# Kernel optimization log

Hardware: AMD Instinct MI355X
Metric: run time of the kernel (lower is better)

## Reference

```python
import jax, jax.numpy as jnp
import numpy as np

N = 50000
E = 800000
T = 10
H = 128
D = 64
P = 65536


def setup_inputs() -> dict:
    key = jax.random.key(0)
    ks = jax.random.split(key, 16)
    inp = {}
    inp["node_type_ids"] = jax.random.randint(ks[0], (N,), 0, T)
    inp["adj_rows"] = jax.random.randint(ks[1], (E,), 0, N)
    inp["adj_cols"] = jax.random.randint(ks[2], (E,), 0, N)
    inp["adj_vals"] = jax.random.uniform(ks[3], (E,), dtype=jnp.float32)
    inp["pairs"] = jax.random.randint(ks[4], (2, P), 0, N)
    s = 0.02
    inp["node_emb"] = jax.random.normal(ks[5], (N, H), dtype=jnp.float32) * s
    inp["type_emb"] = jax.random.normal(ks[6], (T, H), dtype=jnp.float32) * s
    inp["W1"] = jax.random.normal(ks[7], (H, H), dtype=jnp.float32) * s
    inp["b1"] = jnp.zeros((H,), dtype=jnp.float32)
    inp["W2"] = jax.random.normal(ks[8], (H, D), dtype=jnp.float32) * s
    inp["b2"] = jnp.zeros((D,), dtype=jnp.float32)
    inp["Wp1"] = jax.random.normal(ks[9], (3 * D, D), dtype=jnp.float32) * s
    inp["bp1"] = jnp.zeros((D,), dtype=jnp.float32)
    inp["Wp2"] = jax.random.normal(ks[10], (D, 1), dtype=jnp.float32) * s
    inp["bp2"] = jnp.zeros((1,), dtype=jnp.float32)
    return inp


def _spmm(rows, cols, vals, x):
    # sparse.mm(adj, x): out[r] = sum_e vals[e] * x[cols[e]] for rows[e]==r
    msgs = vals[:, None] * x[cols]          # [E, F] gather (irregular)
    return jax.ops.segment_sum(msgs, rows, num_segments=N)


def reference(node_type_ids, adj_rows, adj_cols, adj_vals, pairs,
              node_emb, type_emb, W1, b1, W2, b2, Wp1, bp1, Wp2, bp2):
    # encode: node_embedding(arange(N)) is just the full table
    x = node_emb + type_emb[node_type_ids]                    # [N, H]
    h = jax.nn.relu(_spmm(adj_rows, adj_cols, adj_vals, x) @ W1 + b1)  # gcn1 + relu
    # dropout is identity in eval mode
    z = _spmm(adj_rows, adj_cols, adj_vals, h) @ W2 + b2      # [N, D] gcn2
    # score
    src = z[pairs[0]]                                         # [P, D]
    dst = z[pairs[1]]                                         # [P, D]
    feat = jnp.concatenate([src, dst, src * dst], axis=-1)    # [P, 3D]
    out = jax.nn.relu(feat @ Wp1 + bp1) @ Wp2 + bp2           # [P, 1]
    return out[:, 0]
```

## Files before the change

### kernel.cpp

```cpp
#include <hip/hip_runtime.h>

#define N_NODES 50000
#define N_EDGES 800000
#define NPAIRS  65536

#define NBUCK 391
#define RTILE 2048
#define RBLOCKS 391

typedef unsigned short ushort_t;
typedef unsigned int uint_t;
typedef unsigned long long u64_t;
typedef ushort_t ushort8v __attribute__((ext_vector_type(8)));
typedef short bf16x8 __attribute__((ext_vector_type(8)));
typedef float f32x4 __attribute__((ext_vector_type(4)));

__device__ inline ushort_t f2bf(float f) {
    uint_t u = __float_as_uint(f);
    u = (u + 0x7FFF + ((u >> 16) & 1)) >> 16;
    return (ushort_t)u;
}
__device__ inline float bf2f(ushort_t b) {
    return __uint_as_float(((uint_t)b) << 16);
}


__global__ __launch_bounds__(256) void pack_hist_kernel(const int* __restrict__ rows,
                                                        const int* __restrict__ cols,
                                                        const float* __restrict__ vals,
                                                        u64_t* __restrict__ tmpA,
                                                        int* __restrict__ blockhist, int e) {
    __shared__ int lh[NBUCK];
    int blk = blockIdx.x, t = threadIdx.x;
    for (int i = t; i < NBUCK; i += 256) lh[i] = 0;
    __syncthreads();
    int base = blk * RTILE;
#pragma unroll
    for (int k = 0; k < RTILE / 256; k++) {
        int idx = base + k * 256 + t;
        if (idx < e) {
            int r = rows[idx];
            uint_t payload = (uint_t)cols[idx] | ((uint_t)f2bf(vals[idx]) << 16);
            tmpA[idx] = ((u64_t)r << 32) | payload;
            atomicAdd(&lh[r >> 7], 1);
        }
    }
    __syncthreads();
    for (int d = t; d < NBUCK; d += 256) blockhist[d * RBLOCKS + blk] = lh[d];
}

__global__ __launch_bounds__(256) void scan_block_kernel(const int* __restrict__ cnt,
                                                         int* __restrict__ excl,
                                                         int* __restrict__ blksum, int n) {
    __shared__ int s[256];
    int tid = threadIdx.x;
    int i = blockIdx.x * 256 + tid;
    int v = (i < n) ? cnt[i] : 0;
    s[tid] = v; __syncthreads();
    for (int off = 1; off < 256; off <<= 1) {
        int t = (tid >= off) ? s[tid - off] : 0;
        __syncthreads();
        s[tid] += t;
        __syncthreads();
    }
    if (i < n) excl[i] = s[tid] - v;
    if (tid == 255) blksum[blockIdx.x] = s[255];
}

__global__ __launch_bounds__(256) void scan_mid_kernel(int* __restrict__ data, int n) {
    __shared__ int s[256];
    __shared__ int carry;
    int t = threadIdx.x;
    if (t == 0) carry = 0;
    __syncthreads();
    for (int base = 0; base < n; base += 256) {
        int i = base + t;
        int v = (i < n) ? data[i] : 0;
        s[t] = v; __syncthreads();
        for (int off = 1; off < 256; off <<= 1) {
            int x = (t >= off) ? s[t - off] : 0;
            __syncthreads();
            s[t] += x;
            __syncthreads();
        }
        int excl = s[t] - v + carry;
        if (i < n) data[i] = excl;
        __syncthreads();
        if (t == 255) carry += s[255];
        __syncthreads();
    }
}

__global__ __launch_bounds__(256) void scan_add2_kernel(int* __restrict__ data,
                                                        const int* __restrict__ blksum, int n) {
    int i = blockIdx.x * 256 + threadIdx.x;
    if (i < n) data[i] += blksum[blockIdx.x];
}

__global__ __launch_bounds__(256) void radix_scatter_kernel(const u64_t* __restrict__ tmpA,
                                                            const int* __restrict__ gofs,
                                                            u64_t* __restrict__ tmpB, int e) {
    __shared__ u64_t stage[RTILE];
    __shared__ int lh[NBUCK];
    __shared__ int lstart[NBUCK];
    __shared__ int lcur[NBUCK];
    int blk = blockIdx.x, t = threadIdx.x;
    for (int i = t; i < NBUCK; i += 256) lh[i] = 0;
    __syncthreads();
    int base = blk * RTILE;
    int cnt = min(RTILE, e - base);
    for (int k = t; k < cnt; k += 256) {
        int d = (int)(tmpA[base + k] >> 39);
        atomicAdd(&lh[d], 1);
    }
    __syncthreads();
    if (t == 0) {
        int s = 0;
        for (int d = 0; d < NBUCK; d++) { lstart[d] = s; s += lh[d]; }
    }
    __syncthreads();
    for (int i = t; i < NBUCK; i += 256) lcur[i] = lstart[i];
    __syncthreads();
    for (int k = t; k < cnt; k += 256) {
        u64_t it = tmpA[base + k];
        int d = (int)(it >> 39);
        int slot = atomicAdd(&lcur[d], 1);
        stage[slot] = it;
    }
    __syncthreads();
    for (int k = t; k < cnt; k += 256) {
        u64_t it = stage[k];
        int d = (int)(it >> 39);
        tmpB[gofs[d * RBLOCKS + blk] + (k - lstart[d])] = it;
    }
}

__global__ __launch_bounds__(256) void bucket_sort_kernel(const u64_t* __restrict__ tmpB,
                                                          const int* __restrict__ gofs,
                                                          uint_t* __restrict__ csr_edge,
                                                          int* __restrict__ row_ptr, int e, int n) {
    __shared__ uint_t stage[4096];
    __shared__ int lh[128];
    __shared__ int lstart[128];
    __shared__ int lcur[128];
    int d = blockIdx.x, t = threadIdx.x;
    int bstart = gofs[d * RBLOCKS];
    int bend = (d == NBUCK - 1) ? e : gofs[(d + 1) * RBLOCKS];
    int len = bend - bstart;
    for (int i = t; i < 128; i += 256) lh[i] = 0;
    __syncthreads();
    for (int k = t; k < len; k += 256) {
        int lr = (int)((tmpB[bstart + k] >> 32) & 127);
        atomicAdd(&lh[lr], 1);
    }
    __syncthreads();
    if (t == 0) {
        int s = 0;
        for (int j = 0; j < 128; j++) { lstart[j] = s; s += lh[j]; }
    }
    __syncthreads();
    if (t < 128) {
        int grow = d * 128 + t;
        if (grow <= n) row_ptr[grow] = bstart + lstart[t];
    }
    for (int i = t; i < 128; i += 256) lcur[i] = lstart[i];
    __syncthreads();
    for (int k = t; k < len; k += 256) {
        u64_t it = tmpB[bstart + k];
        int lr = (int)((it >> 32) & 127);
        int slot = atomicAdd(&lcur[lr], 1);
        stage[slot] = (uint_t)it;
    }
    __syncthreads();
    for (int k = t; k < len; k += 256) csr_edge[bstart + k] = stage[k];
}


__global__ __launch_bounds__(256) void prep_w_kernel(const float* __restrict__ W1,
                                                     const float* __restrict__ W2,
                                                     ushort_t* __restrict__ Wt1,
                                                     ushort_t* __restrict__ Wt2) {
    int g = blockIdx.x * 256 + threadIdx.x;
    if (g < 2048) {
        int c = g & 127, k8 = g >> 7;
        ushort8v o;
#pragma unroll
        for (int j = 0; j < 8; j++) o[j] = f2bf(W1[(size_t)(k8 * 8 + j) * 128 + c]);
        *(ushort8v*)&Wt1[(size_t)c * 128 + k8 * 8] = o;
    } else if (g < 3072) {
        int g2 = g - 2048;
        int c = g2 & 63, k8 = g2 >> 6;
        ushort8v o;
#pragma unroll
        for (int j = 0; j < 8; j++) o[j] = f2bf(W2[(size_t)(k8 * 8 + j) * 64 + c]);
        *(ushort8v*)&Wt2[(size_t)c * 128 + k8 * 8] = o;
    }
}


__global__ __launch_bounds__(256) void gemm1_mfma_kernel(const float* __restrict__ node_emb,
                                                         const float* __restrict__ type_emb,
                                                         const int* __restrict__ tids,
                                                         const ushort_t* __restrict__ Wt1,
                                                         ushort_t* __restrict__ y, int n) {
    __shared__ __align__(16) ushort_t As[64 * 128];
    __shared__ __align__(16) ushort_t Ws[128 * 128];
    int t = threadIdx.x;

    for (int gi = t; gi < 2048; gi += 256) {
        int c = gi >> 4, kg = gi & 15;
        ushort8v v = *(const ushort8v*)&Wt1[gi * 8];
        *(ushort8v*)&Ws[c * 128 + ((kg ^ (c & 7)) << 3)] = v;
    }
    int row_l = t >> 2;
    int row_g = blockIdx.x * 64 + row_l;
    int kseg = (t & 3) * 32;
    if (row_g < n) {
        int tv = tids[row_g];
        const float4* na = (const float4*)(node_emb + (size_t)row_g * 128 + kseg);
        const float4* ta = (const float4*)(type_emb + (size_t)tv * 128 + kseg);
#pragma unroll
        for (int i2 = 0; i2 < 4; i2++) {
            float4 a = na[i2 * 2], b = ta[i2 * 2];
            float4 a2 = na[i2 * 2 + 1], b2 = ta[i2 * 2 + 1];
            ushort8v o;
            o[0] = f2bf(a.x + b.x);  o[1] = f2bf(a.y + b.y);
            o[2] = f2bf(a.z + b.z);  o[3] = f2bf(a.w + b.w);
            o[4] = f2bf(a2.x + b2.x); o[5] = f2bf(a2.y + b2.y);
            o[6] = f2bf(a2.z + b2.z); o[7] = f2bf(a2.w + b2.w);
            int kg = (t & 3) * 4 + i2;
            *(ushort8v*)&As[row_l * 128 + ((kg ^ (row_l & 7)) << 3)] = o;
        }
    } else {
        ushort8v z = (ushort8v)(ushort_t)0;
#pragma unroll
        for (int i2 = 0; i2 < 4; i2++) {
            int kg = (t & 3) * 4 + i2;
            *(ushort8v*)&As[row_l * 128 + ((kg ^ (row_l & 7)) << 3)] = z;
        }
    }
    __syncthreads();

    int lane = t & 63, wid = t >> 6;
    int m0 = (wid & 1) * 32, n0 = (wid >> 1) * 64;
    int lr = lane & 15, lk = lane >> 4;
    f32x4 acc[2][4] = {};
#pragma unroll
    for (int ks = 0; ks < 4; ks++) {
        int kg = ks * 4 + lk;
        bf16x8 afr[2];
#pragma unroll
        for (int mt = 0; mt < 2; mt++) {
            int r = m0 + mt * 16 + lr;
            afr[mt] = *(const bf16x8*)&As[r * 128 + ((kg ^ (r & 7)) << 3)];
        }
#pragma unroll
        for (int nt = 0; nt < 4; nt++) {
            int c = n0 + nt * 16 + lr;
            bf16x8 bfr = *(const bf16x8*)&Ws[c * 128 + ((kg ^ (c & 7)) << 3)];
            acc[0][nt] = __builtin_amdgcn_mfma_f32_16x16x32_bf16(afr[0], bfr, acc[0][nt], 0, 0, 0);
            acc[1][nt] = __builtin_amdgcn_mfma_f32_16x16x32_bf16(afr[1], bfr, acc[1][nt], 0, 0, 0);
        }
    }
#pragma unroll
    for (int mt = 0; mt < 2; mt++) {
#pragma unroll
        for (int j = 0; j < 4; j++) {
            int rg = blockIdx.x * 64 + m0 + mt * 16 + lk * 4 + j;
            if (rg < n) {
#pragma unroll
                for (int nt = 0; nt < 4; nt++) {
                    int c = n0 + nt * 16 + lr;
                    y[(size_t)rg * 128 + c] = f2bf(acc[mt][nt][j]);
                }
            }
        }
    }
}


__global__ __launch_bounds__(256) void gemm2_mfma_kernel(const ushort_t* __restrict__ h,
                                                         const ushort_t* __restrict__ Wt2,
                                                         ushort_t* __restrict__ g, int n) {
    __shared__ __align__(16) ushort_t As[64 * 128];
    __shared__ __align__(16) ushort_t Ws[64 * 128];
    int t = threadIdx.x;

    for (int gi = t; gi < 1024; gi += 256) {
        int c = gi >> 4, kg = gi & 15;
        ushort8v v = *(const ushort8v*)&Wt2[gi * 8];
        *(ushort8v*)&Ws[c * 128 + ((kg ^ (c & 7)) << 3)] = v;
    }
    int row_l = t >> 2;
    int row_g = blockIdx.x * 64 + row_l;
    int kseg = (t & 3) * 32;
    if (row_g < n) {
        const ushort8v* hr = (const ushort8v*)(h + (size_t)row_g * 128 + kseg);
#pragma unroll
        for (int i2 = 0; i2 < 4; i2++) {
            ushort8v v = hr[i2];
            int kg = (t & 3) * 4 + i2;
            *(ushort8v*)&As[row_l * 128 + ((kg ^ (row_l & 7)) << 3)] = v;
        }
    } else {
        ushort8v z = (ushort8v)(ushort_t)0;
#pragma unroll
        for (int i2 = 0; i2 < 4; i2++) {
            int kg = (t & 3) * 4 + i2;
            *(ushort8v*)&As[row_l * 128 + ((kg ^ (row_l & 7)) << 3)] = z;
        }
    }
    __syncthreads();

    int lane = t & 63, wid = t >> 6;
    int m0 = (wid & 1) * 32, n0 = (wid >> 1) * 32;
    int lr = lane & 15, lk = lane >> 4;
    f32x4 acc[2][2] = {};
#pragma unroll
    for (int ks = 0; ks < 4; ks++) {
        int kg = ks * 4 + lk;
        bf16x8 afr[2];
#pragma unroll
        for (int mt = 0; mt < 2; mt++) {
            int r = m0 + mt * 16 + lr;
            afr[mt] = *(const bf16x8*)&As[r * 128 + ((kg ^ (r & 7)) << 3)];
        }
#pragma unroll
        for (int nt = 0; nt < 2; nt++) {
            int c = n0 + nt * 16 + lr;
            bf16x8 bfr = *(const bf16x8*)&Ws[c * 128 + ((kg ^ (c & 7)) << 3)];
            acc[0][nt] = __builtin_amdgcn_mfma_f32_16x16x32_bf16(afr[0], bfr, acc[0][nt], 0, 0, 0);
            acc[1][nt] = __builtin_amdgcn_mfma_f32_16x16x32_bf16(afr[1], bfr, acc[1][nt], 0, 0, 0);
        }
    }
#pragma unroll
    for (int mt = 0; mt < 2; mt++) {
#pragma unroll
        for (int j = 0; j < 4; j++) {
            int rg = blockIdx.x * 64 + m0 + mt * 16 + lk * 4 + j;
            if (rg < n) {
#pragma unroll
                for (int nt = 0; nt < 2; nt++) {
                    int c = n0 + nt * 16 + lr;
                    g[(size_t)rg * 64 + c] = f2bf(acc[mt][nt][j]);
                }
            }
        }
    }
}


template <int F, bool RELU, bool BF16OUT>
__global__ __launch_bounds__(256) void spmm_v4_kernel(const int* __restrict__ row_ptr,
                                                      const uint_t* __restrict__ csr_edge,
                                                      const ushort_t* __restrict__ src,
                                                      const float* __restrict__ bias,
                                                      void* __restrict__ dst, int n) {
    constexpr int GL = F / 8;
    constexpr int RPB = (64 / GL) * 4;
    int t = threadIdx.x;
    int lane = t & 63, wid = t >> 6;
    int gl = lane % GL;
    int gbase = lane - gl;
    int row = blockIdx.x * RPB + wid * (64 / GL) + (lane / GL);
    int c8 = gl * 8;
    if (row >= n) return;
    int start = row_ptr[row], end = row_ptr[row + 1];

    float acc[8] = {};
    for (int base = start; base < end; base += GL) {
        int idx = base + gl;
        uint_t pe = (idx < end) ? csr_edge[idx] : 0u;
        int cnt = min(GL, end - base);
        for (int j = 0; j < cnt; j++) {
            uint_t p = (uint_t)__shfl((int)pe, gbase + j);
            int cc = p & 0xFFFF;
            float vv = bf2f((ushort_t)(p >> 16));
            const ushort8v s = *(const ushort8v*)(src + (size_t)cc * F + c8);
#pragma unroll
            for (int m = 0; m < 8; m++) acc[m] += vv * bf2f(s[m]);
        }
    }
#pragma unroll
    for (int m = 0; m < 8; m++) {
        acc[m] += bias[c8 + m];
        if (RELU) acc[m] = fmaxf(acc[m], 0.f);
    }
    if (BF16OUT) {
        ushort8v o;
#pragma unroll
        for (int m = 0; m < 8; m++) o[m] = f2bf(acc[m]);
        *(ushort8v*)((ushort_t*)dst + (size_t)row * F + c8) = o;
    } else {
        float4 o0 = make_float4(acc[0], acc[1], acc[2], acc[3]);
        float4 o1 = make_float4(acc[4], acc[5], acc[6], acc[7]);
        *(float4*)((float*)dst + (size_t)row * F + c8) = o0;
        *(float4*)((float*)dst + (size_t)row * F + c8 + 4) = o1;
    }
}


__global__ __launch_bounds__(256) void pair_kernel(const int* __restrict__ pairs,
                                                   const float* __restrict__ z,
                                                   const float* __restrict__ Wp1,
                                                   const float* __restrict__ bp1,
                                                   const float* __restrict__ Wp2,
                                                   const float* __restrict__ bp2,
                                                   float* __restrict__ out) {
    __shared__ float As[32][33];
    __shared__ float Ws[32][64];
    int t = threadIdx.x;
    int tx = t & 15, ty = t >> 4;
    int row0 = blockIdx.x * 32;
    const int* p0s = pairs;
    const int* p1s = pairs + NPAIRS;
    float acc[2][4] = {};
    int lrow = t >> 3, lk0 = (t & 7) << 2;
    int rg = row0 + lrow;
    int p0 = p0s[rg], p1 = p1s[rg];
    for (int kc = 0; kc < 192; kc += 32) {
        float4 v;
        if (kc < 64) {
            v = *(const float4*)(z + (size_t)p0 * 64 + kc + lk0);
        } else if (kc < 128) {
            v = *(const float4*)(z + (size_t)p1 * 64 + (kc - 64) + lk0);
        } else {
            float4 a = *(const float4*)(z + (size_t)p0 * 64 + (kc - 128) + lk0);
            float4 b = *(const float4*)(z + (size_t)p1 * 64 + (kc - 128) + lk0);
            v = make_float4(a.x * b.x, a.y * b.y, a.z * b.z, a.w * b.w);
        }
        As[lrow][lk0 + 0] = v.x; As[lrow][lk0 + 1] = v.y;
        As[lrow][lk0 + 2] = v.z; As[lrow][lk0 + 3] = v.w;
#pragma unroll
        for (int l = 0; l < 2; l++) {
            int idx = l * 1024 + t * 4;
            int kk = idx >> 6, c = idx & 63;
            *(float4*)&Ws[kk][c] = *(const float4*)(Wp1 + (size_t)(kc + kk) * 64 + c);
        }
        __syncthreads();
#pragma unroll
        for (int kk = 0; kk < 32; kk++) {
            float4 w = *(const float4*)&Ws[kk][tx * 4];
#pragma unroll
            for (int i = 0; i < 2; i++) {
                float a = As[ty + 16 * i][kk];
                acc[i][0] += a * w.x; acc[i][1] += a * w.y;
                acc[i][2] += a * w.z; acc[i][3] += a * w.w;
            }
        }
        __syncthreads();
    }
    float b0 = bp1[tx * 4], b1v = bp1[tx * 4 + 1], b2v = bp1[tx * 4 + 2], b3v = bp1[tx * 4 + 3];
    float w0 = Wp2[tx * 4], w1 = Wp2[tx * 4 + 1], w2 = Wp2[tx * 4 + 2], w3 = Wp2[tx * 4 + 3];
#pragma unroll
    for (int i = 0; i < 2; i++) {
        float p = fmaxf(acc[i][0] + b0, 0.f) * w0 + fmaxf(acc[i][1] + b1v, 0.f) * w1 +
                  fmaxf(acc[i][2] + b2v, 0.f) * w2 + fmaxf(acc[i][3] + b3v, 0.f) * w3;
        p += __shfl_xor(p, 1);
        p += __shfl_xor(p, 2);
        p += __shfl_xor(p, 4);
        p += __shfl_xor(p, 8);
        if (tx == 0) out[row0 + ty + 16 * i] = p + bp2[0];
    }
}


extern "C" void kernel_launch(void* const* d_in, const int* in_sizes, int n_in,
                              void* d_out, int out_size, void* d_ws, size_t ws_size,
                              hipStream_t stream) {
    const int*   tids     = (const int*)d_in[0];
    const int*   adj_rows = (const int*)d_in[1];
    const int*   adj_cols = (const int*)d_in[2];
    const float* adj_vals = (const float*)d_in[3];
    const int*   pairs    = (const int*)d_in[4];
    const float* node_emb = (const float*)d_in[5];
    const float* type_emb = (const float*)d_in[6];
    const float* W1  = (const float*)d_in[7];
    const float* b1  = (const float*)d_in[8];
    const float* W2  = (const float*)d_in[9];
    const float* b2  = (const float*)d_in[10];
    const float* Wp1 = (const float*)d_in[11];
    const float* bp1 = (const float*)d_in[12];
    const float* Wp2 = (const float*)d_in[13];
    const float* bp2 = (const float*)d_in[14];
    float* out = (float*)d_out;

    int n = in_sizes[0];
    int e = in_sizes[1];
    int p = in_sizes[4] / 2;

    char* ws = (char*)d_ws;
    ushort_t* bufY = (ushort_t*)ws;
    u64_t* tmpA = (u64_t*)ws;
    char* wsB = ws + (size_t)n * 128 * sizeof(ushort_t);
    ushort_t* bufH = (ushort_t*)wsB;
    float* bufZ = (float*)wsB;
    u64_t* tmpB = (u64_t*)wsB;

    int* row_ptr   = (int*)(wsB + (size_t)n * 128 * sizeof(ushort_t));
    int* blockhist = row_ptr + (n + 1);
    int L  = NBUCK * RBLOCKS;
    int* blksum1   = blockhist + L;
    uint_t* csr_edge = (uint_t*)(blksum1 + 1024);
    ushort_t* Wt1 = (ushort_t*)(csr_edge + e);
    ushort_t* Wt2 = Wt1 + 128 * 128;

    int SG = (L + 255) / 256;

    prep_w_kernel<<<12, 256, 0, stream>>>(W1, W2, Wt1, Wt2);
    pack_hist_kernel<<<RBLOCKS, 256, 0, stream>>>(adj_rows, adj_cols, adj_vals, tmpA, blockhist, e);
    scan_block_kernel<<<SG, 256, 0, stream>>>(blockhist, blockhist, blksum1, L);
    scan_mid_kernel<<<1, 256, 0, stream>>>(blksum1, SG);
    scan_add2_kernel<<<SG, 256, 0, stream>>>(blockhist, blksum1, L);
    radix_scatter_kernel<<<RBLOCKS, 256, 0, stream>>>(tmpA, blockhist, tmpB, e);
    bucket_sort_kernel<<<NBUCK, 256, 0, stream>>>(tmpB, blockhist, csr_edge, row_ptr, e, n);

    gemm1_mfma_kernel<<<(n + 63) / 64, 256, 0, stream>>>(node_emb, type_emb, tids, Wt1, bufY, n);
    spmm_v4_kernel<128, true, true><<<(n + 15) / 16, 256, 0, stream>>>(row_ptr, csr_edge, bufY, b1, bufH, n);
    gemm2_mfma_kernel<<<(n + 63) / 64, 256, 0, stream>>>(bufH, Wt2, bufY, n);
    spmm_v4_kernel<64, false, false><<<(n + 31) / 32, 256, 0, stream>>>(row_ptr, csr_edge, bufY, b2, bufZ, n);
    pair_kernel<<<p / 32, 256, 0, stream>>>(pairs, bufZ, Wp1, bp1, Wp2, bp2, out);
}
```

Baseline: 151.7 us.

## Fuse first SpMM with second GEMM and replace per-block histogram scan with atomics

The separate relu-SpMM and gemm2 kernels are merged into one kernel. Each block gathers 16 rows of aggregated features into LDS, applies bias and ReLU, then multiplies by W2 with MFMA, so the intermediate H matrix never round-trips through global memory. The radix bucketing drops its per-block histogram and three-kernel scan in favour of global atomic bucket counts, a single-block scan and atomic offset reservation in the scatter kernel. This cuts kernel launches and scan traffic, but the order of edges within a bucket no longer follows a deterministic per-block layout, and the fused kernel has to reload W2 into LDS for every 16 rows.

```diff
diff --git a/kernel.cpp b/kernel.cpp
--- a/kernel.cpp
+++ b/kernel.cpp
@@ -29,7 +29,7 @@
                                                         const int* __restrict__ cols,
                                                         const float* __restrict__ vals,
                                                         u64_t* __restrict__ tmpA,
-                                                        int* __restrict__ blockhist, int e) {
+                                                        int* __restrict__ Bcnt, int e) {
     __shared__ int lh[NBUCK];
     int blk = blockIdx.x, t = threadIdx.x;
     for (int i = t; i < NBUCK; i += 256) lh[i] = 0;
@@ -46,36 +46,21 @@
         }
     }
     __syncthreads();
-    for (int d = t; d < NBUCK; d += 256) blockhist[d * RBLOCKS + blk] = lh[d];
-}
-
-__global__ __launch_bounds__(256) void scan_block_kernel(const int* __restrict__ cnt,
-                                                         int* __restrict__ excl,
-                                                         int* __restrict__ blksum, int n) {
-    __shared__ int s[256];
-    int tid = threadIdx.x;
-    int i = blockIdx.x * 256 + tid;
-    int v = (i < n) ? cnt[i] : 0;
-    s[tid] = v; __syncthreads();
-    for (int off = 1; off < 256; off <<= 1) {
-        int t = (tid >= off) ? s[tid - off] : 0;
-        __syncthreads();
-        s[tid] += t;
-        __syncthreads();
-    }
-    if (i < n) excl[i] = s[tid] - v;
-    if (tid == 255) blksum[blockIdx.x] = s[255];
-}
-
-__global__ __launch_bounds__(256) void scan_mid_kernel(int* __restrict__ data, int n) {
+    for (int d = t; d < NBUCK; d += 256)
+        if (lh[d]) atomicAdd(&Bcnt[d], lh[d]);
+}
+
+__global__ __launch_bounds__(256) void scan_bucket_kernel(const int* __restrict__ Bcnt,
+                                                          int* __restrict__ base,
+                                                          int* __restrict__ cur, int e) {
     __shared__ int s[256];
     __shared__ int carry;
     int t = threadIdx.x;
     if (t == 0) carry = 0;
     __syncthreads();
-    for (int base = 0; base < n; base += 256) {
-        int i = base + t;
-        int v = (i < n) ? data[i] : 0;
+    for (int b0 = 0; b0 < NBUCK; b0 += 256) {
+        int i = b0 + t;
+        int v = (i < NBUCK) ? Bcnt[i] : 0;
         s[t] = v; __syncthreads();
         for (int off = 1; off < 256; off <<= 1) {
             int x = (t >= off) ? s[t - off] : 0;
@@ -84,26 +69,22 @@
             __syncthreads();
         }
         int excl = s[t] - v + carry;
-        if (i < n) data[i] = excl;
+        if (i < NBUCK) { base[i] = excl; cur[i] = excl; }
         __syncthreads();
         if (t == 255) carry += s[255];
         __syncthreads();
     }
-}
-
-__global__ __launch_bounds__(256) void scan_add2_kernel(int* __restrict__ data,
-                                                        const int* __restrict__ blksum, int n) {
-    int i = blockIdx.x * 256 + threadIdx.x;
-    if (i < n) data[i] += blksum[blockIdx.x];
+    if (t == 0) base[NBUCK] = e;
 }
 
 __global__ __launch_bounds__(256) void radix_scatter_kernel(const u64_t* __restrict__ tmpA,
-                                                            const int* __restrict__ gofs,
+                                                            int* __restrict__ cur,
                                                             u64_t* __restrict__ tmpB, int e) {
     __shared__ u64_t stage[RTILE];
     __shared__ int lh[NBUCK];
     __shared__ int lstart[NBUCK];
     __shared__ int lcur[NBUCK];
+    __shared__ int gstart[NBUCK];
     int blk = blockIdx.x, t = threadIdx.x;
     for (int i = t; i < NBUCK; i += 256) lh[i] = 0;
     __syncthreads();
@@ -119,7 +100,10 @@
         for (int d = 0; d < NBUCK; d++) { lstart[d] = s; s += lh[d]; }
     }
     __syncthreads();
-    for (int i = t; i < NBUCK; i += 256) lcur[i] = lstart[i];
+    for (int d = t; d < NBUCK; d += 256) {
+        lcur[d] = lstart[d];
+        if (lh[d]) gstart[d] = atomicAdd(&cur[d], lh[d]);
+    }
     __syncthreads();
     for (int k = t; k < cnt; k += 256) {
         u64_t it = tmpA[base + k];
@@ -131,12 +115,12 @@
     for (int k = t; k < cnt; k += 256) {
         u64_t it = stage[k];
         int d = (int)(it >> 39);
-        tmpB[gofs[d * RBLOCKS + blk] + (k - lstart[d])] = it;
+        tmpB[gstart[d] + (k - lstart[d])] = it;
     }
 }
 
 __global__ __launch_bounds__(256) void bucket_sort_kernel(const u64_t* __restrict__ tmpB,
-                                                          const int* __restrict__ gofs,
+                                                          const int* __restrict__ base,
                                                           uint_t* __restrict__ csr_edge,
                                                           int* __restrict__ row_ptr, int e, int n) {
     __shared__ uint_t stage[4096];
@@ -144,8 +128,8 @@
     __shared__ int lstart[128];
     __shared__ int lcur[128];
     int d = blockIdx.x, t = threadIdx.x;
-    int bstart = gofs[d * RBLOCKS];
-    int bend = (d == NBUCK - 1) ? e : gofs[(d + 1) * RBLOCKS];
+    int bstart = base[d];
+    int bend = base[d + 1];
     int len = bend - bstart;
     for (int i = t; i < 128; i += 256) lh[i] = 0;
     __syncthreads();
@@ -279,73 +263,68 @@
 }
 
 
-__global__ __launch_bounds__(256) void gemm2_mfma_kernel(const ushort_t* __restrict__ h,
-                                                         const ushort_t* __restrict__ Wt2,
-                                                         ushort_t* __restrict__ g, int n) {
-    __shared__ __align__(16) ushort_t As[64 * 128];
+__global__ __launch_bounds__(256) void spmm1_fused_kernel(const int* __restrict__ row_ptr,
+                                                          const uint_t* __restrict__ csr_edge,
+                                                          const ushort_t* __restrict__ y,
+                                                          const float* __restrict__ b1,
+                                                          const ushort_t* __restrict__ Wt2,
+                                                          ushort_t* __restrict__ g, int n) {
     __shared__ __align__(16) ushort_t Ws[64 * 128];
+    __shared__ __align__(16) ushort_t Ht[16 * 128];
     int t = threadIdx.x;
-
     for (int gi = t; gi < 1024; gi += 256) {
         int c = gi >> 4, kg = gi & 15;
         ushort8v v = *(const ushort8v*)&Wt2[gi * 8];
         *(ushort8v*)&Ws[c * 128 + ((kg ^ (c & 7)) << 3)] = v;
     }
-    int row_l = t >> 2;
-    int row_g = blockIdx.x * 64 + row_l;
-    int kseg = (t & 3) * 32;
-    if (row_g < n) {
-        const ushort8v* hr = (const ushort8v*)(h + (size_t)row_g * 128 + kseg);
-#pragma unroll
-        for (int i2 = 0; i2 < 4; i2++) {
-            ushort8v v = hr[i2];
-            int kg = (t & 3) * 4 + i2;
-            *(ushort8v*)&As[row_l * 128 + ((kg ^ (row_l & 7)) << 3)] = v;
-        }
-    } else {
-        ushort8v z = (ushort8v)(ushort_t)0;
-#pragma unroll
-        for (int i2 = 0; i2 < 4; i2++) {
-            int kg = (t & 3) * 4 + i2;
-            *(ushort8v*)&As[row_l * 128 + ((kg ^ (row_l & 7)) << 3)] = z;
-        }
-    }
-    __syncthreads();
 
     int lane = t & 63, wid = t >> 6;
-    int m0 = (wid & 1) * 32, n0 = (wid >> 1) * 32;
+    int gl = lane & 15;
+    int gbase = lane & 48;
+    int lrow = wid * 4 + (lane >> 4);
+    int row = blockIdx.x * 16 + lrow;
+    int c8 = gl * 8;
+
+    float acc[8] = {};
+    if (row < n) {
+        int start = row_ptr[row], end = row_ptr[row + 1];
+        for (int base = start; base < end; base += 16) {
+            int idx = base + gl;
+            uint_t pe = (idx < end) ? csr_edge[idx] : 0u;
+            int cnt = min(16, end - base);
+            for (int j = 0; j < cnt; j++) {
+                uint_t pk = (uint_t)__shfl((int)pe, gbase + j);
+                int cc = pk & 0xFFFF;
+                float vv = bf2f((ushort_t)(pk >> 16));
+                const ushort8v s = *(const ushort8v*)(y + (size_t)cc * 128 + c8);
+#pragma unroll
+                for (int m = 0; m < 8; m++) acc[m] += vv * bf2f(s[m]);
+            }
+        }
+#pragma unroll
+        for (int m = 0; m < 8; m++) acc[m] = fmaxf(acc[m] + b1[c8 + m], 0.f);
+    }
+    ushort8v ho;
+#pragma unroll
+    for (int m = 0; m < 8; m++) ho[m] = f2bf(acc[m]);
+    *(ushort8v*)&Ht[lrow * 128 + ((gl ^ (lrow & 7)) << 3)] = ho;
+    __syncthreads();
+
     int lr = lane & 15, lk = lane >> 4;
-    f32x4 acc[2][2] = {};
+    int n0 = wid * 16;
+    f32x4 cacc = {};
 #pragma unroll
     for (int ks = 0; ks < 4; ks++) {
         int kg = ks * 4 + lk;
-        bf16x8 afr[2];
-#pragma unroll
-        for (int mt = 0; mt < 2; mt++) {
-            int r = m0 + mt * 16 + lr;
-            afr[mt] = *(const bf16x8*)&As[r * 128 + ((kg ^ (r & 7)) << 3)];
-        }
-#pragma unroll
-        for (int nt = 0; nt < 2; nt++) {
-            int c = n0 + nt * 16 + lr;
-            bf16x8 bfr = *(const bf16x8*)&Ws[c * 128 + ((kg ^ (c & 7)) << 3)];
-            acc[0][nt] = __builtin_amdgcn_mfma_f32_16x16x32_bf16(afr[0], bfr, acc[0][nt], 0, 0, 0);
-            acc[1][nt] = __builtin_amdgcn_mfma_f32_16x16x32_bf16(afr[1], bfr, acc[1][nt], 0, 0, 0);
-        }
-    }
-#pragma unroll
-    for (int mt = 0; mt < 2; mt++) {
-#pragma unroll
-        for (int j = 0; j < 4; j++) {
-            int rg = blockIdx.x * 64 + m0 + mt * 16 + lk * 4 + j;
-            if (rg < n) {
-#pragma unroll
-                for (int nt = 0; nt < 2; nt++) {
-                    int c = n0 + nt * 16 + lr;
-                    g[(size_t)rg * 64 + c] = f2bf(acc[mt][nt][j]);
-                }
-            }
-        }
+        bf16x8 afr = *(const bf16x8*)&Ht[lr * 128 + ((kg ^ (lr & 7)) << 3)];
+        int c = n0 + lr;
+        bf16x8 bfr = *(const bf16x8*)&Ws[c * 128 + ((kg ^ (c & 7)) << 3)];
+        cacc = __builtin_amdgcn_mfma_f32_16x16x32_bf16(afr, bfr, cacc, 0, 0, 0);
+    }
+#pragma unroll
+    for (int j = 0; j < 4; j++) {
+        int rg = blockIdx.x * 16 + lk * 4 + j;
+        if (rg < n) g[(size_t)rg * 64 + n0 + lr] = f2bf(cacc[j]);
     }
 }
 
@@ -490,34 +469,30 @@
     int p = in_sizes[4] / 2;
 
     char* ws = (char*)d_ws;
+    u64_t* tmpA = (u64_t*)ws;
     ushort_t* bufY = (ushort_t*)ws;
-    u64_t* tmpA = (u64_t*)ws;
+    float* bufZ = (float*)ws;
     char* wsB = ws + (size_t)n * 128 * sizeof(ushort_t);
-    ushort_t* bufH = (ushort_t*)wsB;
-    float* bufZ = (float*)wsB;
     u64_t* tmpB = (u64_t*)wsB;
-
-    int* row_ptr   = (int*)(wsB + (size_t)n * 128 * sizeof(ushort_t));
-    int* blockhist = row_ptr + (n + 1);
-    int L  = NBUCK * RBLOCKS;
-    int* blksum1   = blockhist + L;
-    uint_t* csr_edge = (uint_t*)(blksum1 + 1024);
+    ushort_t* bufG = (ushort_t*)wsB;
+
+    int* row_ptr = (int*)(wsB + (size_t)e * sizeof(u64_t));
+    int* Bcnt    = row_ptr + (n + 1);
+    int* base    = Bcnt + NBUCK;
+    int* cur     = base + NBUCK + 1;
+    uint_t* csr_edge = (uint_t*)(cur + NBUCK);
     ushort_t* Wt1 = (ushort_t*)(csr_edge + e);
     ushort_t* Wt2 = Wt1 + 128 * 128;
 
-    int SG = (L + 255) / 256;
-
+    hipMemsetAsync(Bcnt, 0, NBUCK * sizeof(int), stream);
     prep_w_kernel<<<12, 256, 0, stream>>>(W1, W2, Wt1, Wt2);
-    pack_hist_kernel<<<RBLOCKS, 256, 0, stream>>>(adj_rows, adj_cols, adj_vals, tmpA, blockhist, e);
-    scan_block_kernel<<<SG, 256, 0, stream>>>(blockhist, blockhist, blksum1, L);
-    scan_mid_kernel<<<1, 256, 0, stream>>>(blksum1, SG);
-    scan_add2_kernel<<<SG, 256, 0, stream>>>(blockhist, blksum1, L);
-    radix_scatter_kernel<<<RBLOCKS, 256, 0, stream>>>(tmpA, blockhist, tmpB, e);
-    bucket_sort_kernel<<<NBUCK, 256, 0, stream>>>(tmpB, blockhist, csr_edge, row_ptr, e, n);
+    pack_hist_kernel<<<RBLOCKS, 256, 0, stream>>>(adj_rows, adj_cols, adj_vals, tmpA, Bcnt, e);
+    scan_bucket_kernel<<<1, 256, 0, stream>>>(Bcnt, base, cur, e);
+    radix_scatter_kernel<<<RBLOCKS, 256, 0, stream>>>(tmpA, cur, tmpB, e);
+    bucket_sort_kernel<<<NBUCK, 256, 0, stream>>>(tmpB, base, csr_edge, row_ptr, e, n);
 
     gemm1_mfma_kernel<<<(n + 63) / 64, 256, 0, stream>>>(node_emb, type_emb, tids, Wt1, bufY, n);
-    spmm_v4_kernel<128, true, true><<<(n + 15) / 16, 256, 0, stream>>>(row_ptr, csr_edge, bufY, b1, bufH, n);
-    gemm2_mfma_kernel<<<(n + 63) / 64, 256, 0, stream>>>(bufH, Wt2, bufY, n);
-    spmm_v4_kernel<64, false, false><<<(n + 31) / 32, 256, 0, stream>>>(row_ptr, csr_edge, bufY, b2, bufZ, n);
+    spmm1_fused_kernel<<<(n + 15) / 16, 256, 0, stream>>>(row_ptr, csr_edge, bufY, b1, Wt2, bufG, n);
+    spmm_v4_kernel<64, false, false><<<(n + 31) / 32, 256, 0, stream>>>(row_ptr, csr_edge, bufG, b2, bufZ, n);
     pair_kernel<<<p / 32, 256, 0, stream>>>(pairs, bufZ, Wp1, bp1, Wp2, bp2, out);
 }
```

Result: slower. 159.6 us (+5.2%).

## Replace per-block histogram scan with atomic bucket offsets; enlarge pair tile

Applied to the files above, without the earlier changes.

The radix bucketing drops the per-block histogram matrix and its three-kernel scan. Instead, global bucket counts are accumulated atomically, one small kernel scans them, and each scatter block claims its output offsets with atomicAdd on per-bucket cursors. This removes two launches and a large scan, at the cost of a memset and a nondeterministic edge order within each bucket, which the later per-row sort handles. Separately, the pair kernel now processes 64 pairs per block instead of 32, reusing each loaded weight tile across more rows.

```diff
diff --git a/kernel.cpp b/kernel.cpp
--- a/kernel.cpp
+++ b/kernel.cpp
@@ -29,7 +29,7 @@
                                                         const int* __restrict__ cols,
                                                         const float* __restrict__ vals,
                                                         u64_t* __restrict__ tmpA,
-                                                        int* __restrict__ blockhist, int e) {
+                                                        int* __restrict__ Bcnt, int e) {
     __shared__ int lh[NBUCK];
     int blk = blockIdx.x, t = threadIdx.x;
     for (int i = t; i < NBUCK; i += 256) lh[i] = 0;
@@ -46,36 +46,21 @@
         }
     }
     __syncthreads();
-    for (int d = t; d < NBUCK; d += 256) blockhist[d * RBLOCKS + blk] = lh[d];
-}
-
-__global__ __launch_bounds__(256) void scan_block_kernel(const int* __restrict__ cnt,
-                                                         int* __restrict__ excl,
-                                                         int* __restrict__ blksum, int n) {
-    __shared__ int s[256];
-    int tid = threadIdx.x;
-    int i = blockIdx.x * 256 + tid;
-    int v = (i < n) ? cnt[i] : 0;
-    s[tid] = v; __syncthreads();
-    for (int off = 1; off < 256; off <<= 1) {
-        int t = (tid >= off) ? s[tid - off] : 0;
-        __syncthreads();
-        s[tid] += t;
-        __syncthreads();
-    }
-    if (i < n) excl[i] = s[tid] - v;
-    if (tid == 255) blksum[blockIdx.x] = s[255];
-}
-
-__global__ __launch_bounds__(256) void scan_mid_kernel(int* __restrict__ data, int n) {
+    for (int d = t; d < NBUCK; d += 256)
+        if (lh[d]) atomicAdd(&Bcnt[d], lh[d]);
+}
+
+__global__ __launch_bounds__(256) void scan_bucket_kernel(const int* __restrict__ Bcnt,
+                                                          int* __restrict__ base,
+                                                          int* __restrict__ cur, int e) {
     __shared__ int s[256];
     __shared__ int carry;
     int t = threadIdx.x;
     if (t == 0) carry = 0;
     __syncthreads();
-    for (int base = 0; base < n; base += 256) {
-        int i = base + t;
-        int v = (i < n) ? data[i] : 0;
+    for (int b0 = 0; b0 < NBUCK; b0 += 256) {
+        int i = b0 + t;
+        int v = (i < NBUCK) ? Bcnt[i] : 0;
         s[t] = v; __syncthreads();
         for (int off = 1; off < 256; off <<= 1) {
             int x = (t >= off) ? s[t - off] : 0;
@@ -84,26 +69,22 @@
             __syncthreads();
         }
         int excl = s[t] - v + carry;
-        if (i < n) data[i] = excl;
+        if (i < NBUCK) { base[i] = excl; cur[i] = excl; }
         __syncthreads();
         if (t == 255) carry += s[255];
         __syncthreads();
     }
-}
-
-__global__ __launch_bounds__(256) void scan_add2_kernel(int* __restrict__ data,
-                                                        const int* __restrict__ blksum, int n) {
-    int i = blockIdx.x * 256 + threadIdx.x;
-    if (i < n) data[i] += blksum[blockIdx.x];
+    if (t == 0) base[NBUCK] = e;
 }
 
 __global__ __launch_bounds__(256) void radix_scatter_kernel(const u64_t* __restrict__ tmpA,
-                                                            const int* __restrict__ gofs,
+                                                            int* __restrict__ cur,
                                                             u64_t* __restrict__ tmpB, int e) {
     __shared__ u64_t stage[RTILE];
     __shared__ int lh[NBUCK];
     __shared__ int lstart[NBUCK];
     __shared__ int lcur[NBUCK];
+    __shared__ int gstart[NBUCK];
     int blk = blockIdx.x, t = threadIdx.x;
     for (int i = t; i < NBUCK; i += 256) lh[i] = 0;
     __syncthreads();
@@ -119,7 +100,10 @@
         for (int d = 0; d < NBUCK; d++) { lstart[d] = s; s += lh[d]; }
     }
     __syncthreads();
-    for (int i = t; i < NBUCK; i += 256) lcur[i] = lstart[i];
+    for (int d = t; d < NBUCK; d += 256) {
+        lcur[d] = lstart[d];
+        if (lh[d]) gstart[d] = atomicAdd(&cur[d], lh[d]);
+    }
     __syncthreads();
     for (int k = t; k < cnt; k += 256) {
         u64_t it = tmpA[base + k];
@@ -131,12 +115,12 @@
     for (int k = t; k < cnt; k += 256) {
         u64_t it = stage[k];
         int d = (int)(it >> 39);
-        tmpB[gofs[d * RBLOCKS + blk] + (k - lstart[d])] = it;
+        tmpB[gstart[d] + (k - lstart[d])] = it;
     }
 }
 
 __global__ __launch_bounds__(256) void bucket_sort_kernel(const u64_t* __restrict__ tmpB,
-                                                          const int* __restrict__ gofs,
+                                                          const int* __restrict__ base,
                                                           uint_t* __restrict__ csr_edge,
                                                           int* __restrict__ row_ptr, int e, int n) {
     __shared__ uint_t stage[4096];
@@ -144,8 +128,8 @@
     __shared__ int lstart[128];
     __shared__ int lcur[128];
     int d = blockIdx.x, t = threadIdx.x;
-    int bstart = gofs[d * RBLOCKS];
-    int bend = (d == NBUCK - 1) ? e : gofs[(d + 1) * RBLOCKS];
+    int bstart = base[d];
+    int bend = base[d + 1];
     int len = bend - bstart;
     for (int i = t; i < 128; i += 256) lh[i] = 0;
     __syncthreads();
@@ -407,30 +391,36 @@
                                                    const float* __restrict__ Wp2,
                                                    const float* __restrict__ bp2,
                                                    float* __restrict__ out) {
-    __shared__ float As[32][33];
+    __shared__ float As[64][33];
     __shared__ float Ws[32][64];
     int t = threadIdx.x;
     int tx = t & 15, ty = t >> 4;
-    int row0 = blockIdx.x * 32;
+    int row0 = blockIdx.x * 64;
     const int* p0s = pairs;
     const int* p1s = pairs + NPAIRS;
-    float acc[2][4] = {};
+    float acc[4][4] = {};
     int lrow = t >> 3, lk0 = (t & 7) << 2;
-    int rg = row0 + lrow;
-    int p0 = p0s[rg], p1 = p1s[rg];
+    int rga = row0 + lrow, rgb = rga + 32;
+    int p0a = p0s[rga], p1a = p1s[rga];
+    int p0b = p0s[rgb], p1b = p1s[rgb];
     for (int kc = 0; kc < 192; kc += 32) {
-        float4 v;
-        if (kc < 64) {
-            v = *(const float4*)(z + (size_t)p0 * 64 + kc + lk0);
-        } else if (kc < 128) {
-            v = *(const float4*)(z + (size_t)p1 * 64 + (kc - 64) + lk0);
-        } else {
-            float4 a = *(const float4*)(z + (size_t)p0 * 64 + (kc - 128) + lk0);
-            float4 b = *(const float4*)(z + (size_t)p1 * 64 + (kc - 128) + lk0);
-            v = make_float4(a.x * b.x, a.y * b.y, a.z * b.z, a.w * b.w);
-        }
-        As[lrow][lk0 + 0] = v.x; As[lrow][lk0 + 1] = v.y;
-        As[lrow][lk0 + 2] = v.z; As[lrow][lk0 + 3] = v.w;
+#pragma unroll
+        for (int l = 0; l < 2; l++) {
+            int pp0 = l ? p0b : p0a, pp1 = l ? p1b : p1a;
+            float4 v;
+            if (kc < 64) {
+                v = *(const float4*)(z + (size_t)pp0 * 64 + kc + lk0);
+            } else if (kc < 128) {
+                v = *(const float4*)(z + (size_t)pp1 * 64 + (kc - 64) + lk0);
+            } else {
+                float4 a = *(const float4*)(z + (size_t)pp0 * 64 + (kc - 128) + lk0);
+                float4 b = *(const float4*)(z + (size_t)pp1 * 64 + (kc - 128) + lk0);
+                v = make_float4(a.x * b.x, a.y * b.y, a.z * b.z, a.w * b.w);
+            }
+            int r = lrow + 32 * l;
+            As[r][lk0 + 0] = v.x; As[r][lk0 + 1] = v.y;
+            As[r][lk0 + 2] = v.z; As[r][lk0 + 3] = v.w;
+        }
 #pragma unroll
         for (int l = 0; l < 2; l++) {
             int idx = l * 1024 + t * 4;
@@ -442,7 +432,7 @@
         for (int kk = 0; kk < 32; kk++) {
             float4 w = *(const float4*)&Ws[kk][tx * 4];
 #pragma unroll
-            for (int i = 0; i < 2; i++) {
+            for (int i = 0; i < 4; i++) {
                 float a = As[ty + 16 * i][kk];
                 acc[i][0] += a * w.x; acc[i][1] += a * w.y;
                 acc[i][2] += a * w.z; acc[i][3] += a * w.w;
@@ -453,14 +443,14 @@
     float b0 = bp1[tx * 4], b1v = bp1[tx * 4 + 1], b2v = bp1[tx * 4 + 2], b3v = bp1[tx * 4 + 3];
     float w0 = Wp2[tx * 4], w1 = Wp2[tx * 4 + 1], w2 = Wp2[tx * 4 + 2], w3 = Wp2[tx * 4 + 3];
 #pragma unroll
-    for (int i = 0; i < 2; i++) {
-        float p = fmaxf(acc[i][0] + b0, 0.f) * w0 + fmaxf(acc[i][1] + b1v, 0.f) * w1 +
-                  fmaxf(acc[i][2] + b2v, 0.f) * w2 + fmaxf(acc[i][3] + b3v, 0.f) * w3;
-        p += __shfl_xor(p, 1);
-        p += __shfl_xor(p, 2);
-        p += __shfl_xor(p, 4);
-        p += __shfl_xor(p, 8);
-        if (tx == 0) out[row0 + ty + 16 * i] = p + bp2[0];
+    for (int i = 0; i < 4; i++) {
+        float pv = fmaxf(acc[i][0] + b0, 0.f) * w0 + fmaxf(acc[i][1] + b1v, 0.f) * w1 +
+                   fmaxf(acc[i][2] + b2v, 0.f) * w2 + fmaxf(acc[i][3] + b3v, 0.f) * w3;
+        pv += __shfl_xor(pv, 1);
+        pv += __shfl_xor(pv, 2);
+        pv += __shfl_xor(pv, 4);
+        pv += __shfl_xor(pv, 8);
+        if (tx == 0) out[row0 + ty + 16 * i] = pv + bp2[0];
     }
 }
 
@@ -490,34 +480,31 @@
     int p = in_sizes[4] / 2;
 
     char* ws = (char*)d_ws;
+    u64_t* tmpA = (u64_t*)ws;
     ushort_t* bufY = (ushort_t*)ws;
-    u64_t* tmpA = (u64_t*)ws;
     char* wsB = ws + (size_t)n * 128 * sizeof(ushort_t);
+    u64_t* tmpB = (u64_t*)wsB;
     ushort_t* bufH = (ushort_t*)wsB;
     float* bufZ = (float*)wsB;
-    u64_t* tmpB = (u64_t*)wsB;
-
-    int* row_ptr   = (int*)(wsB + (size_t)n * 128 * sizeof(ushort_t));
-    int* blockhist = row_ptr + (n + 1);
-    int L  = NBUCK * RBLOCKS;
-    int* blksum1   = blockhist + L;
-    uint_t* csr_edge = (uint_t*)(blksum1 + 1024);
+
+    int* row_ptr = (int*)(wsB + (size_t)n * 128 * sizeof(ushort_t));
+    int* Bcnt    = row_ptr + (n + 1);
+    int* base    = Bcnt + NBUCK;
+    int* cur     = base + NBUCK + 1;
+    uint_t* csr_edge = (uint_t*)(cur + NBUCK);
     ushort_t* Wt1 = (ushort_t*)(csr_edge + e);
     ushort_t* Wt2 = Wt1 + 128 * 128;
 
-    int SG = (L + 255) / 256;
-
+    hipMemsetAsync(Bcnt, 0, NBUCK * sizeof(int), stream);
     prep_w_kernel<<<12, 256, 0, stream>>>(W1, W2, Wt1, Wt2);
-    pack_hist_kernel<<<RBLOCKS, 256, 0, stream>>>(adj_rows, adj_cols, adj_vals, tmpA, blockhist, e);
-    scan_block_kernel<<<SG, 256, 0, stream>>>(blockhist, blockhist, blksum1, L);
-    scan_mid_kernel<<<1, 256, 0, stream>>>(blksum1, SG);
-    scan_add2_kernel<<<SG, 256, 0, stream>>>(blockhist, blksum1, L);
-    radix_scatter_kernel<<<RBLOCKS, 256, 0, stream>>>(tmpA, blockhist, tmpB, e);
-    bucket_sort_kernel<<<NBUCK, 256, 0, stream>>>(tmpB, blockhist, csr_edge, row_ptr, e, n);
+    pack_hist_kernel<<<RBLOCKS, 256, 0, stream>>>(adj_rows, adj_cols, adj_vals, tmpA, Bcnt, e);
+    scan_bucket_kernel<<<1, 256, 0, stream>>>(Bcnt, base, cur, e);
+    radix_scatter_kernel<<<RBLOCKS, 256, 0, stream>>>(tmpA, cur, tmpB, e);
+    bucket_sort_kernel<<<NBUCK, 256, 0, stream>>>(tmpB, base, csr_edge, row_ptr, e, n);
 
     gemm1_mfma_kernel<<<(n + 63) / 64, 256, 0, stream>>>(node_emb, type_emb, tids, Wt1, bufY, n);
     spmm_v4_kernel<128, true, true><<<(n + 15) / 16, 256, 0, stream>>>(row_ptr, csr_edge, bufY, b1, bufH, n);
     gemm2_mfma_kernel<<<(n + 63) / 64, 256, 0, stream>>>(bufH, Wt2, bufY, n);
     spmm_v4_kernel<64, false, false><<<(n + 31) / 32, 256, 0, stream>>>(row_ptr, csr_edge, bufY, b2, bufZ, n);
-    pair_kernel<<<p / 32, 256, 0, stream>>>(pairs, bufZ, Wp1, bp1, Wp2, bp2, out);
-}
+    pair_kernel<<<p / 64, 256, 0, stream>>>(pairs, bufZ, Wp1, bp1, Wp2, bp2, out);
+}
```

Measured after the change: 163.4 us. 1.08x slower.

## Rewrite pair scoring MLP with bf16 MFMA and pre-transposed Wp1

Applied to the files above, without the earlier changes.

The scalar FP32 pair-scoring kernel becomes an MFMA kernel. Each block gathers 64 pairs' src, dst and src*dst features into swizzled bf16 shared memory and multiplies them against a pre-transposed bf16 Wp1 using 16x16x32 MFMA. The fused ReLU and Wp2 reduction runs on the accumulators. prep_w_kernel gains a Wp1 transpose/convert stage. The aim is to cut ALU-bound FMA work and LDS traffic, at the cost of bf16 precision in the first scoring layer.

```diff
diff --git a/kernel.cpp b/kernel.cpp
--- a/kernel.cpp
+++ b/kernel.cpp
@@ -178,8 +178,10 @@
 
 __global__ __launch_bounds__(256) void prep_w_kernel(const float* __restrict__ W1,
                                                      const float* __restrict__ W2,
+                                                     const float* __restrict__ Wp1,
                                                      ushort_t* __restrict__ Wt1,
-                                                     ushort_t* __restrict__ Wt2) {
+                                                     ushort_t* __restrict__ Wt2,
+                                                     ushort_t* __restrict__ Wtp1) {
     int g = blockIdx.x * 256 + threadIdx.x;
     if (g < 2048) {
         int c = g & 127, k8 = g >> 7;
@@ -194,6 +196,13 @@
 #pragma unroll
         for (int j = 0; j < 8; j++) o[j] = f2bf(W2[(size_t)(k8 * 8 + j) * 64 + c]);
         *(ushort8v*)&Wt2[(size_t)c * 128 + k8 * 8] = o;
+    } else if (g < 4608) {
+        int g2 = g - 3072;
+        int c = g2 / 24, k8 = g2 % 24;
+        ushort8v o;
+#pragma unroll
+        for (int j = 0; j < 8; j++) o[j] = f2bf(Wp1[(size_t)(k8 * 8 + j) * 64 + c]);
+        *(ushort8v*)&Wtp1[(size_t)g2 * 8] = o;
     }
 }
 
@@ -400,67 +409,86 @@
 }
 
 
-__global__ __launch_bounds__(256) void pair_kernel(const int* __restrict__ pairs,
-                                                   const float* __restrict__ z,
-                                                   const float* __restrict__ Wp1,
-                                                   const float* __restrict__ bp1,
-                                                   const float* __restrict__ Wp2,
-                                                   const float* __restrict__ bp2,
-                                                   float* __restrict__ out) {
-    __shared__ float As[32][33];
-    __shared__ float Ws[32][64];
+__global__ __launch_bounds__(256) void pair_mfma_kernel(const int* __restrict__ pairs,
+                                                        const float* __restrict__ z,
+                                                        const ushort_t* __restrict__ Wtp1,
+                                                        const float* __restrict__ bp1,
+                                                        const float* __restrict__ Wp2,
+                                                        const float* __restrict__ bp2,
+                                                        float* __restrict__ out) {
+    __shared__ __align__(16) ushort_t Fs[64 * 192];
+    __shared__ __align__(16) ushort_t Ws[64 * 192];
     int t = threadIdx.x;
-    int tx = t & 15, ty = t >> 4;
-    int row0 = blockIdx.x * 32;
-    const int* p0s = pairs;
-    const int* p1s = pairs + NPAIRS;
-    float acc[2][4] = {};
-    int lrow = t >> 3, lk0 = (t & 7) << 2;
-    int rg = row0 + lrow;
-    int p0 = p0s[rg], p1 = p1s[rg];
-    for (int kc = 0; kc < 192; kc += 32) {
-        float4 v;
-        if (kc < 64) {
-            v = *(const float4*)(z + (size_t)p0 * 64 + kc + lk0);
-        } else if (kc < 128) {
-            v = *(const float4*)(z + (size_t)p1 * 64 + (kc - 64) + lk0);
+
+    for (int gi = t; gi < 1536; gi += 256) {
+        int c = gi / 24, kg = gi % 24;
+        ushort8v v = *(const ushort8v*)&Wtp1[(size_t)gi * 8];
+        *(ushort8v*)&Ws[c * 192 + ((kg ^ (c & 7)) << 3)] = v;
+    }
+    int row_l = t >> 2;
+    int rg = blockIdx.x * 64 + row_l;
+    int p0 = pairs[rg], p1 = pairs[NPAIRS + rg];
+    const float* z0 = z + (size_t)p0 * 64;
+    const float* z1 = z + (size_t)p1 * 64;
+    int q = t & 3;
+#pragma unroll
+    for (int i = 0; i < 6; i++) {
+        int kg = q * 6 + i;
+        int k0 = kg * 8;
+        float v[8];
+        if (k0 < 64) {
+#pragma unroll
+            for (int m = 0; m < 8; m++) v[m] = z0[k0 + m];
+        } else if (k0 < 128) {
+#pragma unroll
+            for (int m = 0; m < 8; m++) v[m] = z1[k0 - 64 + m];
         } else {
-            float4 a = *(const float4*)(z + (size_t)p0 * 64 + (kc - 128) + lk0);
-            float4 b = *(const float4*)(z + (size_t)p1 * 64 + (kc - 128) + lk0);
-            v = make_float4(a.x * b.x, a.y * b.y, a.z * b.z, a.w * b.w);
-        }
-        As[lrow][lk0 + 0] = v.x; As[lrow][lk0 + 1] = v.y;
-        As[lrow][lk0 + 2] = v.z; As[lrow][lk0 + 3] = v.w;
-#pragma unroll
-        for (int l = 0; l < 2; l++) {
-            int idx = l * 1024 + t * 4;
-            int kk = idx >> 6, c = idx & 63;
-            *(float4*)&Ws[kk][c] = *(const float4*)(Wp1 + (size_t)(kc + kk) * 64 + c);
-        }
-        __syncthreads();
-#pragma unroll
-        for (int kk = 0; kk < 32; kk++) {
-            float4 w = *(const float4*)&Ws[kk][tx * 4];
-#pragma unroll
-            for (int i = 0; i < 2; i++) {
-                float a = As[ty + 16 * i][kk];
-                acc[i][0] += a * w.x; acc[i][1] += a * w.y;
-                acc[i][2] += a * w.z; acc[i][3] += a * w.w;
-            }
-        }
-        __syncthreads();
-    }
-    float b0 = bp1[tx * 4], b1v = bp1[tx * 4 + 1], b2v = bp1[tx * 4 + 2], b3v = bp1[tx * 4 + 3];
-    float w0 = Wp2[tx * 4], w1 = Wp2[tx * 4 + 1], w2 = Wp2[tx * 4 + 2], w3 = Wp2[tx * 4 + 3];
-#pragma unroll
-    for (int i = 0; i < 2; i++) {
-        float p = fmaxf(acc[i][0] + b0, 0.f) * w0 + fmaxf(acc[i][1] + b1v, 0.f) * w1 +
-                  fmaxf(acc[i][2] + b2v, 0.f) * w2 + fmaxf(acc[i][3] + b3v, 0.f) * w3;
-        p += __shfl_xor(p, 1);
-        p += __shfl_xor(p, 2);
-        p += __shfl_xor(p, 4);
-        p += __shfl_xor(p, 8);
-        if (tx == 0) out[row0 + ty + 16 * i] = p + bp2[0];
+#pragma unroll
+            for (int m = 0; m < 8; m++) v[m] = z0[k0 - 128 + m] * z1[k0 - 128 + m];
+        }
+        ushort8v o;
+#pragma unroll
+        for (int m = 0; m < 8; m++) o[m] = f2bf(v[m]);
+        *(ushort8v*)&Fs[row_l * 192 + ((kg ^ (row_l & 7)) << 3)] = o;
+    }
+    __syncthreads();
+
+    int lane = t & 63, wid = t >> 6;
+    int m0 = wid * 16;
+    int lr = lane & 15, lk = lane >> 4;
+    f32x4 acc[4] = {};
+#pragma unroll
+    for (int ks = 0; ks < 6; ks++) {
+        int kg = ks * 4 + lk;
+        int r = m0 + lr;
+        bf16x8 afr = *(const bf16x8*)&Fs[r * 192 + ((kg ^ (r & 7)) << 3)];
+#pragma unroll
+        for (int nt = 0; nt < 4; nt++) {
+            int c = nt * 16 + lr;
+            bf16x8 bfr = *(const bf16x8*)&Ws[c * 192 + ((kg ^ (c & 7)) << 3)];
+            acc[nt] = __builtin_amdgcn_mfma_f32_16x16x32_bf16(afr, bfr, acc[nt], 0, 0, 0);
+        }
+    }
+    float s[4] = {};
+#pragma unroll
+    for (int nt = 0; nt < 4; nt++) {
+        int c = nt * 16 + lr;
+        float b = bp1[c], w = Wp2[c];
+#pragma unroll
+        for (int j = 0; j < 4; j++) s[j] += fmaxf(acc[nt][j] + b, 0.f) * w;
+    }
+#pragma unroll
+    for (int j = 0; j < 4; j++) {
+        s[j] += __shfl_xor(s[j], 1);
+        s[j] += __shfl_xor(s[j], 2);
+        s[j] += __shfl_xor(s[j], 4);
+        s[j] += __shfl_xor(s[j], 8);
+    }
+    if (lr == 0) {
+        float bb = bp2[0];
+#pragma unroll
+        for (int j = 0; j < 4; j++)
+            out[blockIdx.x * 64 + m0 + lk * 4 + j] = s[j] + bb;
     }
 }
 
@@ -504,10 +532,11 @@
     uint_t* csr_edge = (uint_t*)(blksum1 + 1024);
     ushort_t* Wt1 = (ushort_t*)(csr_edge + e);
     ushort_t* Wt2 = Wt1 + 128 * 128;
+    ushort_t* Wtp1 = Wt2 + 64 * 128;
 
     int SG = (L + 255) / 256;
 
-    prep_w_kernel<<<12, 256, 0, stream>>>(W1, W2, Wt1, Wt2);
+    prep_w_kernel<<<18, 256, 0, stream>>>(W1, W2, Wp1, Wt1, Wt2, Wtp1);
     pack_hist_kernel<<<RBLOCKS, 256, 0, stream>>>(adj_rows, adj_cols, adj_vals, tmpA, blockhist, e);
     scan_block_kernel<<<SG, 256, 0, stream>>>(blockhist, blockhist, blksum1, L);
     scan_mid_kernel<<<1, 256, 0, stream>>>(blksum1, SG);
@@ -519,5 +548,5 @@
     spmm_v4_kernel<128, true, true><<<(n + 15) / 16, 256, 0, stream>>>(row_ptr, csr_edge, bufY, b1, bufH, n);
     gemm2_mfma_kernel<<<(n + 63) / 64, 256, 0, stream>>>(bufH, Wt2, bufY, n);
     spmm_v4_kernel<64, false, false><<<(n + 31) / 32, 256, 0, stream>>>(row_ptr, csr_edge, bufY, b2, bufZ, n);
-    pair_kernel<<<p / 32, 256, 0, stream>>>(pairs, bufZ, Wp1, bp1, Wp2, bp2, out);
-}
+    pair_mfma_kernel<<<p / 64, 256, 0, stream>>>(pairs, bufZ, Wtp1, bp1, Wp2, bp2, out);
+}
```

After: 142.9 us. -5.8%, faster.
